# Performance work log

Hardware: AMD Instinct MI355X
Metric: run time of the kernel (lower is better)

## Reference

```python
import jax, jax.numpy as jnp
import numpy as np

N_NODES = 100000
N_EDGES = 1600000
IN_CH = 64
OUT_CH = 32
HEADS = 4
NEG_SLOPE = 0.2


def setup_inputs() -> dict:
    key = jax.random.key(0)
    k = jax.random.split(key, 6)
    x = jax.random.normal(k[0], (N_NODES, IN_CH), dtype=jnp.float32)
    edge_index = jax.random.randint(k[1], (2, N_EDGES), 0, N_NODES, dtype=jnp.int32)
    W = jax.random.normal(k[2], (IN_CH, HEADS * OUT_CH), dtype=jnp.float32) * 0.1
    att_src = jax.random.normal(k[3], (1, HEADS, OUT_CH), dtype=jnp.float32) * 0.1
    att_dst = jax.random.normal(k[4], (1, HEADS, OUT_CH), dtype=jnp.float32) * 0.1
    bias = jnp.zeros((HEADS * OUT_CH,), dtype=jnp.float32)
    return {"x": x, "edge_index": edge_index, "W": W,
            "att_src": att_src, "att_dst": att_dst, "bias": bias}


def reference(x, edge_index, W, att_src, att_dst, bias):
    N = x.shape[0]
    H, C = att_src.shape[1], att_src.shape[2]
    # GATConv defaults: add self loops
    loop = jnp.arange(N, dtype=edge_index.dtype)
    src = jnp.concatenate([edge_index[0], loop])  # [E+N]
    dst = jnp.concatenate([edge_index[1], loop])  # [E+N]
    # linear transform -> [N, H, C]
    h = (x @ W).reshape(N, H, C)
    # per-node attention halves: [N, H]
    a_src = jnp.sum(h * att_src, axis=-1)
    a_dst = jnp.sum(h * att_dst, axis=-1)
    # edge scores with LeakyReLU: [E+N, H]
    e = jax.nn.leaky_relu(a_src[src] + a_dst[dst], negative_slope=NEG_SLOPE)
    # segment softmax over destination nodes (numerically stable)
    m = jax.ops.segment_max(e, dst, num_segments=N)           # [N, H]
    m = jnp.where(jnp.isfinite(m), m, 0.0)
    ex = jnp.exp(e - m[dst])                                   # [E+N, H]
    denom = jax.ops.segment_sum(ex, dst, num_segments=N)      # [N, H]
    alpha = ex / (denom[dst] + 1e-16)                          # [E+N, H]
    # scatter-aggregate weighted source features -> [N, H, C]
    out = jax.ops.segment_sum(h[src] * alpha[:, :, None], dst, num_segments=N)
    out = out.reshape(N, H * C) + bias
    return jax.nn.log_softmax(out, axis=1)
```

## Files before the change

### kernel.cpp

```cpp
#include <hip/hip_runtime.h>
#include <hip/hip_bf16.h>

#define IN_CH 64
#define HC 128
#define NHEAD 4
#define NEG 0.2f
#define CAPB 64
#define NB 250
#define BWID 400
#define CAP2 8192
#define CH1 4096
#define VPT 8

typedef short s16x8 __attribute__((ext_vector_type(8)));
typedef float f32x4 __attribute__((ext_vector_type(4)));

__device__ __forceinline__ float leaky(float v) { return fmaxf(v, NEG * v); }
__device__ __forceinline__ unsigned short f2bf(float f) {
    unsigned int u = __float_as_uint(f);
    u += 0x7fff + ((u >> 16) & 1);
    return (unsigned short)(u >> 16);
}
__device__ __forceinline__ float4 add4(float4 a, float4 b) {
    return make_float4(a.x + b.x, a.y + b.y, a.z + b.z, a.w + b.w);
}
__device__ __forceinline__ float4 leaky4(float4 v) {
    return make_float4(leaky(v.x), leaky(v.y), leaky(v.z), leaky(v.w));
}
__device__ __forceinline__ float4 exp4(float4 v) {
    return make_float4(__expf(v.x), __expf(v.y), __expf(v.z), __expf(v.w));
}
__device__ __forceinline__ float comp4(float4 v, int i) {
    float r = v.x;
    r = (i == 1) ? v.y : r;
    r = (i == 2) ? v.z : r;
    r = (i == 3) ? v.w : r;
    return r;
}

__global__ void __launch_bounds__(256) k_xform(
        const float* __restrict__ x, const float* __restrict__ W,
        const float* __restrict__ att_src, const float* __restrict__ att_dst,
        unsigned short* __restrict__ h_bf, float* __restrict__ a_src,
        float* __restrict__ a_dst, int* __restrict__ bcnt, int N) {
    __shared__ unsigned short xs[128][72];
    __shared__ unsigned short wt[144][72];
    const int t = threadIdx.x;
    const int rowbase_blk = blockIdx.x * 128;

    if (blockIdx.x == 0) {
        for (int i = t; i < NB * 16; i += 256) bcnt[i] = 0;
    }

    for (int idx = t; idx < (IN_CH * HC) / 4; idx += 256) {
        const float4 v = ((const float4*)W)[idx];
        const int k = idx >> 5;
        const int c0 = (idx & 31) * 4;
        wt[c0 + 0][k] = f2bf(v.x);
        wt[c0 + 1][k] = f2bf(v.y);
        wt[c0 + 2][k] = f2bf(v.z);
        wt[c0 + 3][k] = f2bf(v.w);
    }
    for (int idx = t; idx < 16 * 64; idx += 256) {
        const int j = idx >> 6, k = idx & 63;
        float v = 0.f;
        if (j < 8) {
            const int h = j & 3;
            const float* att = (j < 4) ? att_src : att_dst;
#pragma unroll
            for (int c = 0; c < 32; ++c)
                v += W[k * HC + h * 32 + c] * att[h * 32 + c];
        }
        wt[128 + j][k] = f2bf(v);
    }
    for (int idx = t; idx < (128 * IN_CH) / 4; idx += 256) {
        const int row = idx >> 4;
        const int c0 = (idx & 15) * 4;
        const int grow = min(rowbase_blk + row, N - 1);
        const float4 v = ((const float4*)(x + (size_t)grow * IN_CH))[idx & 15];
        const unsigned int p0 = (unsigned int)f2bf(v.x) | ((unsigned int)f2bf(v.y) << 16);
        const unsigned int p1 = (unsigned int)f2bf(v.z) | ((unsigned int)f2bf(v.w) << 16);
        *(uint2*)&xs[row][c0] = make_uint2(p0, p1);
    }
    __syncthreads();

    const int lane = t & 63;
    const int w = t >> 6;
    const int rbase = w * 32;
    const int lr = lane & 15, lq = lane >> 4;

    f32x4 acc[2][9];
#pragma unroll
    for (int m = 0; m < 2; ++m)
#pragma unroll
        for (int n = 0; n < 9; ++n) acc[m][n] = (f32x4){0.f, 0.f, 0.f, 0.f};

#pragma unroll
    for (int ks = 0; ks < 2; ++ks) {
        const s16x8 a0 = *(const s16x8*)&xs[rbase + lr][ks * 32 + lq * 8];
        const s16x8 a1 = *(const s16x8*)&xs[rbase + 16 + lr][ks * 32 + lq * 8];
#pragma unroll
        for (int n = 0; n < 9; ++n) {
            const s16x8 b = *(const s16x8*)&wt[n * 16 + lr][ks * 32 + lq * 8];
            acc[0][n] = __builtin_amdgcn_mfma_f32_16x16x32_bf16(a0, b, acc[0][n], 0, 0, 0);
            acc[1][n] = __builtin_amdgcn_mfma_f32_16x16x32_bf16(a1, b, acc[1][n], 0, 0, 0);
        }
    }

#pragma unroll
    for (int m = 0; m < 2; ++m) {
#pragma unroll
        for (int j = 0; j < 4; ++j) {
            const int grow = rowbase_blk + rbase + m * 16 + lq * 4 + j;
            if (grow >= N) continue;
#pragma unroll
            for (int n = 0; n < 8; ++n)
                h_bf[(size_t)grow * HC + n * 16 + lr] = f2bf(acc[m][n][j]);
            const float av = acc[m][8][j];
            if (lr < 4) a_src[grow * NHEAD + lr] = av;
            else if (lr < 8) a_dst[grow * NHEAD + (lr - 4)] = av;
        }
    }
}

__global__ void __launch_bounds__(512) k_bin(
        const int* __restrict__ src, const int* __restrict__ dst,
        int* __restrict__ bcnt, int* __restrict__ pairs, int E) {
    __shared__ int hist[NB];
    __shared__ int scanbuf[256];
    __shared__ int startb[NB];
    __shared__ int gbase[NB];
    __shared__ int lbuf[CH1];
    __shared__ int gposb[CH1];

    const int t = threadIdx.x;
    const int base = blockIdx.x * CH1;
    const int cnt = min(CH1, E - base);

    for (int i = t; i < NB; i += 512) hist[i] = 0;
    __syncthreads();

    int pk[VPT]; int rb[VPT];
#pragma unroll
    for (int k = 0; k < VPT; ++k) {
        const int idx = base + k * 512 + t;
        if (idx < E) {
            const int s = src[idx], d = dst[idx];
            const int b = d / BWID;
            const int dl = d - b * BWID;
            pk[k] = (dl << 17) | s;
            const int rank = atomicAdd(&hist[b], 1);
            rb[k] = (b << 16) | rank;
        } else {
            pk[k] = 0; rb[k] = -1;
        }
    }
    __syncthreads();

    if (t < 256) scanbuf[t] = (t < NB) ? hist[t] : 0;
    __syncthreads();
    for (int off = 1; off < 256; off <<= 1) {
        int add = 0;
        if (t < 256 && t >= off) add = scanbuf[t - off];
        __syncthreads();
        if (t < 256) scanbuf[t] += add;
        __syncthreads();
    }
    if (t < NB) {
        const int h = hist[t];
        startb[t] = scanbuf[t] - h;
        gbase[t] = (h > 0) ? atomicAdd(&bcnt[t * 16], h) : 0;
    }
    __syncthreads();

#pragma unroll
    for (int k = 0; k < VPT; ++k) {
        if (rb[k] >= 0) {
            const int b = rb[k] >> 16;
            const int rank = rb[k] & 0xffff;
            const int lpos = startb[b] + rank;
            const int gp = gbase[b] + rank;
            lbuf[lpos] = pk[k];
            gposb[lpos] = (gp < CAP2) ? (b * CAP2 + gp) : -1;
        }
    }
    __syncthreads();

    for (int i = t; i < cnt; i += 512) {
        const int g = gposb[i];
        if (g >= 0) pairs[g] = lbuf[i];
    }
}

__global__ void __launch_bounds__(512) k_fill(
        const int* __restrict__ bcnt, const int* __restrict__ pairs,
        int* __restrict__ srcbuf, int* __restrict__ rowstart,
        int* __restrict__ deg) {
    const int b = blockIdx.x;
    const int t = threadIdx.x;
    __shared__ int scnt[BWID];
    __shared__ int sstart[BWID];
    __shared__ int cur[BWID];
    __shared__ int scan2[512];
    __shared__ int slist[CAP2];
    __shared__ int sbase;

    int part = 0;
    for (int i = t; i < b; i += 512) part += min(bcnt[i * 16], CAP2);
    scan2[t] = part; __syncthreads();
    for (int off = 256; off > 0; off >>= 1) {
        if (t < off) scan2[t] += scan2[t + off];
        __syncthreads();
    }
    if (t == 0) sbase = scan2[0];

    for (int i = t; i < BWID; i += 512) scnt[i] = 0;
    __syncthreads();

    const int mc = min(bcnt[b * 16], CAP2);
    const int pb = b * CAP2;

    for (int i = t; i < mc; i += 512)
        atomicAdd(&scnt[pairs[pb + i] >> 17], 1);
    __syncthreads();

    scan2[t] = (t < BWID) ? scnt[t] : 0;
    __syncthreads();
    for (int off = 1; off < 512; off <<= 1) {
        const int add = (t >= off) ? scan2[t - off] : 0;
        __syncthreads();
        scan2[t] += add;
        __syncthreads();
    }
    if (t < BWID) {
        const int ex = scan2[t] - scnt[t];
        sstart[t] = ex; cur[t] = ex;
        rowstart[b * BWID + t] = sbase + ex;
        deg[b * BWID + t] = scnt[t];
    }
    __syncthreads();

    for (int i = t; i < mc; i += 512) {
        const int e = pairs[pb + i];
        const int p = atomicAdd(&cur[e >> 17], 1);
        slist[p] = e & 0x1ffff;
    }
    __syncthreads();

    for (int i = t; i < mc; i += 512) srcbuf[sbase + i] = slist[i];
}

__global__ void __launch_bounds__(256) k_node(
        const int* __restrict__ deg_, const int* __restrict__ rowstart,
        const int* __restrict__ srcbuf,
        const float* __restrict__ a_src, const float* __restrict__ a_dst,
        const unsigned short* __restrict__ h_bf, const float* __restrict__ bias,
        float* __restrict__ out, int N) {
    const int slot = threadIdx.x >> 4;
    const int l = threadIdx.x & 15;
    int n = blockIdx.x * 16 + slot;
    n = min(n, N - 1);
    const int deg = deg_[n];
    const int start = rowstart[n];
    const int dcap = min(deg, CAPB);

    __shared__ float s_ex[16][CAPB][NHEAD];
    __shared__ int   s_src[16][CAPB];

    const float4 ad4  = *(const float4*)(a_dst + n * NHEAD);
    const float4 asn4 = *(const float4*)(a_src + n * NHEAD);

    float4 sum4 = make_float4(0.f, 0.f, 0.f, 0.f);
    for (int j = l; j < dcap; j += 16) {
        const int s = srcbuf[start + j];
        s_src[slot][j] = s;
        const float4 a = *(const float4*)(a_src + s * NHEAD);
        const float4 e4 = exp4(leaky4(add4(a, ad4)));
        *(float4*)&s_ex[slot][j][0] = e4;
        sum4 = add4(sum4, e4);
    }
    for (int j = CAPB + l; j < deg; j += 16) {
        const int s = srcbuf[start + j];
        const float4 a = *(const float4*)(a_src + s * NHEAD);
        sum4 = add4(sum4, exp4(leaky4(add4(a, ad4))));
    }
#pragma unroll
    for (int off = 1; off < 16; off <<= 1) {
        sum4.x += __shfl_xor(sum4.x, off, 64);
        sum4.y += __shfl_xor(sum4.y, off, 64);
        sum4.z += __shfl_xor(sum4.z, off, 64);
        sum4.w += __shfl_xor(sum4.w, off, 64);
    }
    const float4 self4 = exp4(leaky4(add4(asn4, ad4)));
    sum4 = add4(sum4, self4);
    const float4 r4 = make_float4(1.f / (sum4.x + 1e-16f), 1.f / (sum4.y + 1e-16f),
                                  1.f / (sum4.z + 1e-16f), 1.f / (sum4.w + 1e-16f));

    __builtin_amdgcn_wave_barrier();

    const int hd = l >> 2;
    const float rsel = comp4(r4, hd);
    const float adh  = comp4(ad4, hd);
    float acc[8];
#pragma unroll
    for (int k = 0; k < 8; ++k) acc[k] = 0.f;

    for (int j = 0; j < dcap; ++j) {
        const int s = s_src[slot][j];
        const float al = s_ex[slot][j][hd];
        const uint4 hv = *(const uint4*)(h_bf + (size_t)s * HC + l * 8);
        acc[0] = fmaf(al, __uint_as_float(hv.x << 16), acc[0]);
        acc[1] = fmaf(al, __uint_as_float(hv.x & 0xffff0000u), acc[1]);
        acc[2] = fmaf(al, __uint_as_float(hv.y << 16), acc[2]);
        acc[3] = fmaf(al, __uint_as_float(hv.y & 0xffff0000u), acc[3]);
        acc[4] = fmaf(al, __uint_as_float(hv.z << 16), acc[4]);
        acc[5] = fmaf(al, __uint_as_float(hv.z & 0xffff0000u), acc[5]);
        acc[6] = fmaf(al, __uint_as_float(hv.w << 16), acc[6]);
        acc[7] = fmaf(al, __uint_as_float(hv.w & 0xffff0000u), acc[7]);
    }
    for (int j = CAPB; j < deg; ++j) {
        const int s = srcbuf[start + j];
        const float al = __expf(leaky(a_src[s * NHEAD + hd] + adh));
        const uint4 hv = *(const uint4*)(h_bf + (size_t)s * HC + l * 8);
        acc[0] = fmaf(al, __uint_as_float(hv.x << 16), acc[0]);
        acc[1] = fmaf(al, __uint_as_float(hv.x & 0xffff0000u), acc[1]);
        acc[2] = fmaf(al, __uint_as_float(hv.y << 16), acc[2]);
        acc[3] = fmaf(al, __uint_as_float(hv.y & 0xffff0000u), acc[3]);
        acc[4] = fmaf(al, __uint_as_float(hv.z << 16), acc[4]);
        acc[5] = fmaf(al, __uint_as_float(hv.z & 0xffff0000u), acc[5]);
        acc[6] = fmaf(al, __uint_as_float(hv.w << 16), acc[6]);
        acc[7] = fmaf(al, __uint_as_float(hv.w & 0xffff0000u), acc[7]);
    }
    {
        const float als = comp4(self4, hd);
        const uint4 hv = *(const uint4*)(h_bf + (size_t)n * HC + l * 8);
        acc[0] = fmaf(als, __uint_as_float(hv.x << 16), acc[0]);
        acc[1] = fmaf(als, __uint_as_float(hv.x & 0xffff0000u), acc[1]);
        acc[2] = fmaf(als, __uint_as_float(hv.y << 16), acc[2]);
        acc[3] = fmaf(als, __uint_as_float(hv.y & 0xffff0000u), acc[3]);
        acc[4] = fmaf(als, __uint_as_float(hv.z << 16), acc[4]);
        acc[5] = fmaf(als, __uint_as_float(hv.z & 0xffff0000u), acc[5]);
        acc[6] = fmaf(als, __uint_as_float(hv.w << 16), acc[6]);
        acc[7] = fmaf(als, __uint_as_float(hv.w & 0xffff0000u), acc[7]);
    }

    const float4 b0 = *(const float4*)(bias + l * 8);
    const float4 b1 = *(const float4*)(bias + l * 8 + 4);
    acc[0] = acc[0] * rsel + b0.x; acc[1] = acc[1] * rsel + b0.y;
    acc[2] = acc[2] * rsel + b0.z; acc[3] = acc[3] * rsel + b0.w;
    acc[4] = acc[4] * rsel + b1.x; acc[5] = acc[5] * rsel + b1.y;
    acc[6] = acc[6] * rsel + b1.z; acc[7] = acc[7] * rsel + b1.w;

    float mxv = fmaxf(fmaxf(fmaxf(acc[0], acc[1]), fmaxf(acc[2], acc[3])),
                      fmaxf(fmaxf(acc[4], acc[5]), fmaxf(acc[6], acc[7])));
#pragma unroll
    for (int off = 1; off < 16; off <<= 1) mxv = fmaxf(mxv, __shfl_xor(mxv, off, 64));
    float se = 0.f;
#pragma unroll
    for (int k = 0; k < 8; ++k) se += __expf(acc[k] - mxv);
#pragma unroll
    for (int off = 1; off < 16; off <<= 1) se += __shfl_xor(se, off, 64);
    const float lse = mxv + __logf(se);

    float* op = out + (size_t)n * HC + l * 8;
    *(float4*)op = make_float4(acc[0] - lse, acc[1] - lse, acc[2] - lse, acc[3] - lse);
    *(float4*)(op + 4) = make_float4(acc[4] - lse, acc[5] - lse, acc[6] - lse, acc[7] - lse);
}

extern "C" void kernel_launch(void* const* d_in, const int* in_sizes, int n_in,
                              void* d_out, int out_size, void* d_ws, size_t ws_size,
                              hipStream_t stream) {
    const float* x       = (const float*)d_in[0];
    const int*   ei      = (const int*)d_in[1];
    const float* W       = (const float*)d_in[2];
    const float* att_src = (const float*)d_in[3];
    const float* att_dst = (const float*)d_in[4];
    const float* bias    = (const float*)d_in[5];
    float* out = (float*)d_out;

    const int N = in_sizes[0] / IN_CH;
    const int E = in_sizes[1] / 2;
    const int* src = ei;
    const int* dst = ei + E;

    char* wsb = (char*)d_ws;
    unsigned short* h_bf = (unsigned short*)wsb;    wsb += (size_t)N * HC * 2;
    float* a_src  = (float*)wsb;                    wsb += (size_t)N * NHEAD * 4;
    float* a_dst  = (float*)wsb;                    wsb += (size_t)N * NHEAD * 4;
    int*   bcnt   = (int*)wsb;                      wsb += (size_t)NB * 16 * 4;
    int*   pairs  = (int*)wsb;                      wsb += (size_t)NB * CAP2 * 4;
    int*   srcbuf = (int*)wsb;                      wsb += (size_t)E * 4;
    int*   rowstart = (int*)wsb;                    wsb += (size_t)N * 4;
    int*   deg    = (int*)wsb;                      wsb += (size_t)N * 4;

    k_xform<<<(N + 127) / 128, 256, 0, stream>>>(x, W, att_src, att_dst,
                                                 h_bf, a_src, a_dst, bcnt, N);
    k_bin<<<(E + CH1 - 1) / CH1, 512, 0, stream>>>(src, dst, bcnt, pairs, E);
    k_fill<<<NB, 512, 0, stream>>>(bcnt, pairs, srcbuf, rowstart, deg);
    k_node<<<(N + 15) / 16, 256, 0, stream>>>(deg, rowstart, srcbuf,
                                              a_src, a_dst,
                                              (const unsigned short*)h_bf, bias, out, N);
}
```

Measured before the change: 211.2 us.

## Fuse transform and edge-binning kernels into one launch; recompute edge weights in aggregation

Merges the node feature transform (MFMA GEMM) and the edge binning pass into a single kernel. Blocks are interleaved two transform blocks to one binning block and share a shared-memory union, so the two independent stages can overlap on the GPU. Zeroing of the bin counters moves to a hipMemsetAsync. In the node aggregation kernel, the per-edge exp weights are no longer cached in shared memory; they are recomputed from a_src during the gather, and the loop is unrolled by two to overlap loads. This cuts LDS usage and raises occupancy, at the cost of extra exp work and extra a_src loads.

```diff
diff --git a/kernel.cpp b/kernel.cpp
--- a/kernel.cpp
+++ b/kernel.cpp
@@ -38,157 +38,159 @@
     return r;
 }
 
-__global__ void __launch_bounds__(256) k_xform(
+#define ACC8(al, hv)                                                  \
+    do {                                                              \
+        acc[0] = fmaf((al), __uint_as_float((hv).x << 16), acc[0]);   \
+        acc[1] = fmaf((al), __uint_as_float((hv).x & 0xffff0000u), acc[1]); \
+        acc[2] = fmaf((al), __uint_as_float((hv).y << 16), acc[2]);   \
+        acc[3] = fmaf((al), __uint_as_float((hv).y & 0xffff0000u), acc[3]); \
+        acc[4] = fmaf((al), __uint_as_float((hv).z << 16), acc[4]);   \
+        acc[5] = fmaf((al), __uint_as_float((hv).z & 0xffff0000u), acc[5]); \
+        acc[6] = fmaf((al), __uint_as_float((hv).w << 16), acc[6]);   \
+        acc[7] = fmaf((al), __uint_as_float((hv).w & 0xffff0000u), acc[7]); \
+    } while (0)
+
+__global__ void __launch_bounds__(512, 4) k_front(
         const float* __restrict__ x, const float* __restrict__ W,
         const float* __restrict__ att_src, const float* __restrict__ att_dst,
         unsigned short* __restrict__ h_bf, float* __restrict__ a_src,
-        float* __restrict__ a_dst, int* __restrict__ bcnt, int N) {
-    __shared__ unsigned short xs[128][72];
-    __shared__ unsigned short wt[144][72];
+        float* __restrict__ a_dst,
+        const int* __restrict__ src, const int* __restrict__ dst,
+        int* __restrict__ bcnt, int* __restrict__ pairs,
+        int E, int N, int NXB) {
+    __shared__ union {
+        struct { unsigned short xs[128][72]; unsigned short wt[144][72]; } xf;
+        struct { int hist[NB]; int scanbuf[256]; int startb[NB]; int gbase[NB];
+                 int lbuf[CH1]; int gposb[CH1]; } bn;
+    } sm;
     const int t = threadIdx.x;
-    const int rowbase_blk = blockIdx.x * 128;
-
-    if (blockIdx.x == 0) {
-        for (int i = t; i < NB * 16; i += 256) bcnt[i] = 0;
-    }
-
-    for (int idx = t; idx < (IN_CH * HC) / 4; idx += 256) {
-        const float4 v = ((const float4*)W)[idx];
-        const int k = idx >> 5;
-        const int c0 = (idx & 31) * 4;
-        wt[c0 + 0][k] = f2bf(v.x);
-        wt[c0 + 1][k] = f2bf(v.y);
-        wt[c0 + 2][k] = f2bf(v.z);
-        wt[c0 + 3][k] = f2bf(v.w);
-    }
-    for (int idx = t; idx < 16 * 64; idx += 256) {
-        const int j = idx >> 6, k = idx & 63;
-        float v = 0.f;
-        if (j < 8) {
-            const int h = j & 3;
-            const float* att = (j < 4) ? att_src : att_dst;
-#pragma unroll
-            for (int c = 0; c < 32; ++c)
-                v += W[k * HC + h * 32 + c] * att[h * 32 + c];
-        }
-        wt[128 + j][k] = f2bf(v);
-    }
-    for (int idx = t; idx < (128 * IN_CH) / 4; idx += 256) {
-        const int row = idx >> 4;
-        const int c0 = (idx & 15) * 4;
-        const int grow = min(rowbase_blk + row, N - 1);
-        const float4 v = ((const float4*)(x + (size_t)grow * IN_CH))[idx & 15];
-        const unsigned int p0 = (unsigned int)f2bf(v.x) | ((unsigned int)f2bf(v.y) << 16);
-        const unsigned int p1 = (unsigned int)f2bf(v.z) | ((unsigned int)f2bf(v.w) << 16);
-        *(uint2*)&xs[row][c0] = make_uint2(p0, p1);
-    }
-    __syncthreads();
-
-    const int lane = t & 63;
-    const int w = t >> 6;
-    const int rbase = w * 32;
-    const int lr = lane & 15, lq = lane >> 4;
-
-    f32x4 acc[2][9];
-#pragma unroll
-    for (int m = 0; m < 2; ++m)
-#pragma unroll
-        for (int n = 0; n < 9; ++n) acc[m][n] = (f32x4){0.f, 0.f, 0.f, 0.f};
-
-#pragma unroll
-    for (int ks = 0; ks < 2; ++ks) {
-        const s16x8 a0 = *(const s16x8*)&xs[rbase + lr][ks * 32 + lq * 8];
-        const s16x8 a1 = *(const s16x8*)&xs[rbase + 16 + lr][ks * 32 + lq * 8];
-#pragma unroll
-        for (int n = 0; n < 9; ++n) {
-            const s16x8 b = *(const s16x8*)&wt[n * 16 + lr][ks * 32 + lq * 8];
-            acc[0][n] = __builtin_amdgcn_mfma_f32_16x16x32_bf16(a0, b, acc[0][n], 0, 0, 0);
-            acc[1][n] = __builtin_amdgcn_mfma_f32_16x16x32_bf16(a1, b, acc[1][n], 0, 0, 0);
-        }
-    }
-
-#pragma unroll
-    for (int m = 0; m < 2; ++m) {
+    const int r3 = blockIdx.x % 3;
+
+    if (r3 < 2) {
+        const int xb = (blockIdx.x / 3) * 2 + r3;
+        if (xb >= NXB) return;
+        const int rowbase_blk = xb * 128;
+
+        for (int idx = t; idx < (IN_CH * HC) / 4; idx += 512) {
+            const float4 v = ((const float4*)W)[idx];
+            const int k = idx >> 5;
+            const int c0 = (idx & 31) * 4;
+            sm.xf.wt[c0 + 0][k] = f2bf(v.x);
+            sm.xf.wt[c0 + 1][k] = f2bf(v.y);
+            sm.xf.wt[c0 + 2][k] = f2bf(v.z);
+            sm.xf.wt[c0 + 3][k] = f2bf(v.w);
+        }
+        for (int idx = t; idx < 16 * 64; idx += 512) {
+            const int j = idx >> 6, k = idx & 63;
+            float v = 0.f;
+            if (j < 8) {
+                const int h = j & 3;
+                const float* att = (j < 4) ? att_src : att_dst;
+#pragma unroll
+                for (int c = 0; c < 32; ++c)
+                    v += W[k * HC + h * 32 + c] * att[h * 32 + c];
+            }
+            sm.xf.wt[128 + j][k] = f2bf(v);
+        }
+        for (int idx = t; idx < (128 * IN_CH) / 4; idx += 512) {
+            const int row = idx >> 4;
+            const int c0 = (idx & 15) * 4;
+            const int grow = min(rowbase_blk + row, N - 1);
+            const float4 v = ((const float4*)(x + (size_t)grow * IN_CH))[idx & 15];
+            const unsigned int p0 = (unsigned int)f2bf(v.x) | ((unsigned int)f2bf(v.y) << 16);
+            const unsigned int p1 = (unsigned int)f2bf(v.z) | ((unsigned int)f2bf(v.w) << 16);
+            *(uint2*)&sm.xf.xs[row][c0] = make_uint2(p0, p1);
+        }
+        __syncthreads();
+
+        const int lane = t & 63;
+        const int w = t >> 6;
+        const int rbase = w * 16;
+        const int lr = lane & 15, lq = lane >> 4;
+
+        f32x4 acc[9];
+#pragma unroll
+        for (int n = 0; n < 9; ++n) acc[n] = (f32x4){0.f, 0.f, 0.f, 0.f};
+
+#pragma unroll
+        for (int ks = 0; ks < 2; ++ks) {
+            const s16x8 a0 = *(const s16x8*)&sm.xf.xs[rbase + lr][ks * 32 + lq * 8];
+#pragma unroll
+            for (int n = 0; n < 9; ++n) {
+                const s16x8 b = *(const s16x8*)&sm.xf.wt[n * 16 + lr][ks * 32 + lq * 8];
+                acc[n] = __builtin_amdgcn_mfma_f32_16x16x32_bf16(a0, b, acc[n], 0, 0, 0);
+            }
+        }
+
 #pragma unroll
         for (int j = 0; j < 4; ++j) {
-            const int grow = rowbase_blk + rbase + m * 16 + lq * 4 + j;
+            const int grow = rowbase_blk + rbase + lq * 4 + j;
             if (grow >= N) continue;
 #pragma unroll
             for (int n = 0; n < 8; ++n)
-                h_bf[(size_t)grow * HC + n * 16 + lr] = f2bf(acc[m][n][j]);
-            const float av = acc[m][8][j];
+                h_bf[(size_t)grow * HC + n * 16 + lr] = f2bf(acc[n][j]);
+            const float av = acc[8][j];
             if (lr < 4) a_src[grow * NHEAD + lr] = av;
             else if (lr < 8) a_dst[grow * NHEAD + (lr - 4)] = av;
         }
-    }
-}
-
-__global__ void __launch_bounds__(512) k_bin(
-        const int* __restrict__ src, const int* __restrict__ dst,
-        int* __restrict__ bcnt, int* __restrict__ pairs, int E) {
-    __shared__ int hist[NB];
-    __shared__ int scanbuf[256];
-    __shared__ int startb[NB];
-    __shared__ int gbase[NB];
-    __shared__ int lbuf[CH1];
-    __shared__ int gposb[CH1];
-
-    const int t = threadIdx.x;
-    const int base = blockIdx.x * CH1;
-    const int cnt = min(CH1, E - base);
-
-    for (int i = t; i < NB; i += 512) hist[i] = 0;
-    __syncthreads();
-
-    int pk[VPT]; int rb[VPT];
-#pragma unroll
-    for (int k = 0; k < VPT; ++k) {
-        const int idx = base + k * 512 + t;
-        if (idx < E) {
-            const int s = src[idx], d = dst[idx];
-            const int b = d / BWID;
-            const int dl = d - b * BWID;
-            pk[k] = (dl << 17) | s;
-            const int rank = atomicAdd(&hist[b], 1);
-            rb[k] = (b << 16) | rank;
-        } else {
-            pk[k] = 0; rb[k] = -1;
-        }
-    }
-    __syncthreads();
-
-    if (t < 256) scanbuf[t] = (t < NB) ? hist[t] : 0;
-    __syncthreads();
-    for (int off = 1; off < 256; off <<= 1) {
-        int add = 0;
-        if (t < 256 && t >= off) add = scanbuf[t - off];
-        __syncthreads();
-        if (t < 256) scanbuf[t] += add;
-        __syncthreads();
-    }
-    if (t < NB) {
-        const int h = hist[t];
-        startb[t] = scanbuf[t] - h;
-        gbase[t] = (h > 0) ? atomicAdd(&bcnt[t * 16], h) : 0;
-    }
-    __syncthreads();
-
-#pragma unroll
-    for (int k = 0; k < VPT; ++k) {
-        if (rb[k] >= 0) {
-            const int b = rb[k] >> 16;
-            const int rank = rb[k] & 0xffff;
-            const int lpos = startb[b] + rank;
-            const int gp = gbase[b] + rank;
-            lbuf[lpos] = pk[k];
-            gposb[lpos] = (gp < CAP2) ? (b * CAP2 + gp) : -1;
-        }
-    }
-    __syncthreads();
-
-    for (int i = t; i < cnt; i += 512) {
-        const int g = gposb[i];
-        if (g >= 0) pairs[g] = lbuf[i];
+    } else {
+        const int bb = blockIdx.x / 3;
+        const int base = bb * CH1;
+        const int cnt = min(CH1, E - base);
+
+        for (int i = t; i < NB; i += 512) sm.bn.hist[i] = 0;
+        __syncthreads();
+
+        int pk[VPT]; int rb[VPT];
+#pragma unroll
+        for (int k = 0; k < VPT; ++k) {
+            const int idx = base + k * 512 + t;
+            if (idx < E) {
+                const int s = src[idx], d = dst[idx];
+                const int b = d / BWID;
+                const int dl = d - b * BWID;
+                pk[k] = (dl << 17) | s;
+                const int rank = atomicAdd(&sm.bn.hist[b], 1);
+                rb[k] = (b << 16) | rank;
+            } else {
+                pk[k] = 0; rb[k] = -1;
+            }
+        }
+        __syncthreads();
+
+        if (t < 256) sm.bn.scanbuf[t] = (t < NB) ? sm.bn.hist[t] : 0;
+        __syncthreads();
+        for (int off = 1; off < 256; off <<= 1) {
+            int add = 0;
+            if (t < 256 && t >= off) add = sm.bn.scanbuf[t - off];
+            __syncthreads();
+            if (t < 256) sm.bn.scanbuf[t] += add;
+            __syncthreads();
+        }
+        if (t < NB) {
+            const int h = sm.bn.hist[t];
+            sm.bn.startb[t] = sm.bn.scanbuf[t] - h;
+            sm.bn.gbase[t] = (h > 0) ? atomicAdd(&bcnt[t * 16], h) : 0;
+        }
+        __syncthreads();
+
+#pragma unroll
+        for (int k = 0; k < VPT; ++k) {
+            if (rb[k] >= 0) {
+                const int b = rb[k] >> 16;
+                const int rank = rb[k] & 0xffff;
+                const int lpos = sm.bn.startb[b] + rank;
+                const int gp = sm.bn.gbase[b] + rank;
+                sm.bn.lbuf[lpos] = pk[k];
+                sm.bn.gposb[lpos] = (gp < CAP2) ? (b * CAP2 + gp) : -1;
+            }
+        }
+        __syncthreads();
+
+        for (int i = t; i < cnt; i += 512) {
+            const int g = sm.bn.gposb[i];
+            if (g >= 0) pairs[g] = sm.bn.lbuf[i];
+        }
     }
 }
 
@@ -264,8 +266,7 @@
     const int start = rowstart[n];
     const int dcap = min(deg, CAPB);
 
-    __shared__ float s_ex[16][CAPB][NHEAD];
-    __shared__ int   s_src[16][CAPB];
+    __shared__ int s_src[16][CAPB];
 
     const float4 ad4  = *(const float4*)(a_dst + n * NHEAD);
     const float4 asn4 = *(const float4*)(a_src + n * NHEAD);
@@ -275,9 +276,7 @@
         const int s = srcbuf[start + j];
         s_src[slot][j] = s;
         const float4 a = *(const float4*)(a_src + s * NHEAD);
-        const float4 e4 = exp4(leaky4(add4(a, ad4)));
-        *(float4*)&s_ex[slot][j][0] = e4;
-        sum4 = add4(sum4, e4);
+        sum4 = add4(sum4, exp4(leaky4(add4(a, ad4))));
     }
     for (int j = CAPB + l; j < deg; j += 16) {
         const int s = srcbuf[start + j];
@@ -293,55 +292,47 @@
     }
     const float4 self4 = exp4(leaky4(add4(asn4, ad4)));
     sum4 = add4(sum4, self4);
-    const float4 r4 = make_float4(1.f / (sum4.x + 1e-16f), 1.f / (sum4.y + 1e-16f),
-                                  1.f / (sum4.z + 1e-16f), 1.f / (sum4.w + 1e-16f));
+    const float4 r4v = make_float4(1.f / (sum4.x + 1e-16f), 1.f / (sum4.y + 1e-16f),
+                                   1.f / (sum4.z + 1e-16f), 1.f / (sum4.w + 1e-16f));
 
     __builtin_amdgcn_wave_barrier();
 
     const int hd = l >> 2;
-    const float rsel = comp4(r4, hd);
+    const float rsel = comp4(r4v, hd);
     const float adh  = comp4(ad4, hd);
     float acc[8];
 #pragma unroll
     for (int k = 0; k < 8; ++k) acc[k] = 0.f;
 
-    for (int j = 0; j < dcap; ++j) {
-        const int s = s_src[slot][j];
-        const float al = s_ex[slot][j][hd];
-        const uint4 hv = *(const uint4*)(h_bf + (size_t)s * HC + l * 8);
-        acc[0] = fmaf(al, __uint_as_float(hv.x << 16), acc[0]);
-        acc[1] = fmaf(al, __uint_as_float(hv.x & 0xffff0000u), acc[1]);
-        acc[2] = fmaf(al, __uint_as_float(hv.y << 16), acc[2]);
-        acc[3] = fmaf(al, __uint_as_float(hv.y & 0xffff0000u), acc[3]);
-        acc[4] = fmaf(al, __uint_as_float(hv.z << 16), acc[4]);
-        acc[5] = fmaf(al, __uint_as_float(hv.z & 0xffff0000u), acc[5]);
-        acc[6] = fmaf(al, __uint_as_float(hv.w << 16), acc[6]);
-        acc[7] = fmaf(al, __uint_as_float(hv.w & 0xffff0000u), acc[7]);
-    }
-    for (int j = CAPB; j < deg; ++j) {
-        const int s = srcbuf[start + j];
+    int j = 0;
+    for (; j + 2 <= dcap; j += 2) {
+        const int s0 = s_src[slot][j];
+        const int s1 = s_src[slot][j + 1];
+        const float a0 = a_src[s0 * NHEAD + hd];
+        const float a1 = a_src[s1 * NHEAD + hd];
+        const uint4 h0 = *(const uint4*)(h_bf + (size_t)s0 * HC + l * 8);
+        const uint4 h1 = *(const uint4*)(h_bf + (size_t)s1 * HC + l * 8);
+        const float al0 = __expf(leaky(a0 + adh));
+        const float al1 = __expf(leaky(a1 + adh));
+        ACC8(al0, h0);
+        ACC8(al1, h1);
+    }
+    if (j < dcap) {
+        const int s0 = s_src[slot][j];
+        const float al0 = __expf(leaky(a_src[s0 * NHEAD + hd] + adh));
+        const uint4 h0 = *(const uint4*)(h_bf + (size_t)s0 * HC + l * 8);
+        ACC8(al0, h0);
+    }
+    for (int jj = CAPB; jj < deg; ++jj) {
+        const int s = srcbuf[start + jj];
         const float al = __expf(leaky(a_src[s * NHEAD + hd] + adh));
         const uint4 hv = *(const uint4*)(h_bf + (size_t)s * HC + l * 8);
-        acc[0] = fmaf(al, __uint_as_float(hv.x << 16), acc[0]);
-        acc[1] = fmaf(al, __uint_as_float(hv.x & 0xffff0000u), acc[1]);
-        acc[2] = fmaf(al, __uint_as_float(hv.y << 16), acc[2]);
-        acc[3] = fmaf(al, __uint_as_float(hv.y & 0xffff0000u), acc[3]);
-        acc[4] = fmaf(al, __uint_as_float(hv.z << 16), acc[4]);
-        acc[5] = fmaf(al, __uint_as_float(hv.z & 0xffff0000u), acc[5]);
-        acc[6] = fmaf(al, __uint_as_float(hv.w << 16), acc[6]);
-        acc[7] = fmaf(al, __uint_as_float(hv.w & 0xffff0000u), acc[7]);
+        ACC8(al, hv);
     }
     {
         const float als = comp4(self4, hd);
         const uint4 hv = *(const uint4*)(h_bf + (size_t)n * HC + l * 8);
-        acc[0] = fmaf(als, __uint_as_float(hv.x << 16), acc[0]);
-        acc[1] = fmaf(als, __uint_as_float(hv.x & 0xffff0000u), acc[1]);
-        acc[2] = fmaf(als, __uint_as_float(hv.y << 16), acc[2]);
-        acc[3] = fmaf(als, __uint_as_float(hv.y & 0xffff0000u), acc[3]);
-        acc[4] = fmaf(als, __uint_as_float(hv.z << 16), acc[4]);
-        acc[5] = fmaf(als, __uint_as_float(hv.z & 0xffff0000u), acc[5]);
-        acc[6] = fmaf(als, __uint_as_float(hv.w << 16), acc[6]);
-        acc[7] = fmaf(als, __uint_as_float(hv.w & 0xffff0000u), acc[7]);
+        ACC8(als, hv);
     }
 
     const float4 b0 = *(const float4*)(bias + l * 8);
@@ -393,9 +384,14 @@
     int*   rowstart = (int*)wsb;                    wsb += (size_t)N * 4;
     int*   deg    = (int*)wsb;                      wsb += (size_t)N * 4;
 
-    k_xform<<<(N + 127) / 128, 256, 0, stream>>>(x, W, att_src, att_dst,
-                                                 h_bf, a_src, a_dst, bcnt, N);
-    k_bin<<<(E + CH1 - 1) / CH1, 512, 0, stream>>>(src, dst, bcnt, pairs, E);
+    const int NXB = (N + 127) / 128;
+    const int NBB = (E + CH1 - 1) / CH1;
+
+    hipMemsetAsync(bcnt, 0, (size_t)NB * 16 * 4, stream);
+
+    k_front<<<NBB * 3, 512, 0, stream>>>(x, W, att_src, att_dst,
+                                         h_bf, a_src, a_dst,
+                                         src, dst, bcnt, pairs, E, N, NXB);
     k_fill<<<NB, 512, 0, stream>>>(bcnt, pairs, srcbuf, rowstart, deg);
     k_node<<<(N + 15) / 16, 256, 0, stream>>>(deg, rowstart, srcbuf,
                                               a_src, a_dst,
```

New measurement: 208.8 us. About the same (-1.1%).
